# Kernel optimization log

Hardware: AMD Instinct MI355X
Metric: run time of the kernel (lower is better)

Reference implementation:

```python
import jax, jax.numpy as jnp
import numpy as np

ETA = 1.0
C_STAB = 0.1
SIGMA2 = 512.0  # RBF bandwidth, kernel_args['sigma2']
N_SAMPLE, S, D = 8192, 64, 512


def rbf_kernel(x, sigma2):
    # K[i,j] = exp(-||x_i - x_j||^2 / (2*sigma2)); x: [n, d] -> K: [n, n]
    sq = jnp.sum(x * x, axis=1)
    d2 = sq[:, None] + sq[None, :] - 2.0 * (x @ x.T)
    return jnp.exp(-d2 / (2.0 * sigma2))


def setup_inputs() -> dict:
    key = jax.random.key(0)
    k1, k2, k3 = jax.random.split(key, 3)
    return {
        "input_data": jax.random.normal(k1, (N_SAMPLE, D), dtype=jnp.float32),
        "weight": jax.random.normal(k2, (N_SAMPLE, S), dtype=jnp.float32),
        "inv_lambda_diag": jax.random.normal(k3, (S,), dtype=jnp.float32),
    }


def reference(input_data, weight, inv_lambda_diag):
    K = rbf_kernel(input_data, SIGMA2)          # [n, n]
    E = weight.T @ K                             # [s, n] : e_j for all samples at once
    # loss1 = sum_i e_i^T diag(inv_lambda) e_i, scaled
    loss1 = -jnp.sum(inv_lambda_diag[:, None] * E * E) / (2.0 * ETA ** 2)
    # loss2 = trace(W^T K W) = sum_{s,n} E[s,n] * W[n,s]
    loss2 = jnp.einsum("sn,ns->", E, weight) / (2.0 * ETA)
    L = loss1 + loss2
    return L + (C_STAB / 2.0) * jnp.square(L)
```

## Files before the change

### kernel.cpp

```cpp
#include <hip/hip_runtime.h>
#include <hip/hip_bf16.h>

typedef __bf16 bf16x8 __attribute__((ext_vector_type(8)));
typedef float f32x4 __attribute__((ext_vector_type(4)));
typedef long longx2 __attribute__((ext_vector_type(2)));

#define N 8192
#define D 512
#define NS 64

#define XS_OFF 0
#define WT_OFF (4 * 1024 * 1024)
#define SQ_OFF (WT_OFF + 1024 * 1024)
#define EP_OFF (SQ_OFF + 32 * 1024)
#define SC_OFF (EP_OFF + 8 * 64 * 8192 * 4)

__global__ __launch_bounds__(256) void prep(const float* __restrict__ X,
                                            const float* __restrict__ W,
                                            unsigned char* __restrict__ Xs,
                                            float* __restrict__ sq,
                                            __bf16* __restrict__ WTs,
                                            float* __restrict__ Sacc) {
    __shared__ float T[64][65];
    int t = threadIdx.x;
    if (blockIdx.x == 0 && t == 0) {
        Sacc[0] = 0.f; Sacc[1] = 0.f; ((int*)Sacc)[2] = 0;
    }
    if (blockIdx.x < 2048) {
        int row = blockIdx.x * 4 + (t >> 6);
        int l = t & 63;
        const float* src = X + (size_t)row * D + l * 8;
        float4 v0 = *(const float4*)src;
        float4 v1 = *(const float4*)(src + 4);
        int w0 = __builtin_amdgcn_cvt_pk_fp8_f32(v0.x, v0.y, 0, false);
        w0     = __builtin_amdgcn_cvt_pk_fp8_f32(v0.z, v0.w, w0, true);
        int w1 = __builtin_amdgcn_cvt_pk_fp8_f32(v1.x, v1.y, 0, false);
        w1     = __builtin_amdgcn_cvt_pk_fp8_f32(v1.z, v1.w, w1, true);
        int g = l >> 3, kh = (l >> 2) & 1, q = l & 3;
        int pos = g * 64 + q * 16 + kh * 8;
        uint2 pk = make_uint2((unsigned)w0, (unsigned)w1);
        *(uint2*)(Xs + (size_t)row * 512 + pos) = pk;
        float acc = v0.x*v0.x + v0.y*v0.y + v0.z*v0.z + v0.w*v0.w
                  + v1.x*v1.x + v1.y*v1.y + v1.z*v1.z + v1.w*v1.w;
        for (int off = 32; off > 0; off >>= 1) acc += __shfl_down(acc, off);
        if (l == 0) sq[row] = acc;
    } else {
        int i0 = (blockIdx.x - 2048) * 64;
        for (int j = 0; j < 16; ++j) {
            int idx = t + 256 * j;
            T[idx & 63][idx >> 6] = W[(size_t)(i0 + (idx >> 6)) * NS + (idx & 63)];
        }
        __syncthreads();
        for (int h = 0; h < 2; ++h)
            for (int j = 0; j < 8; ++j) {
                int idx = t + 256 * j;
                int s = idx >> 5, il = idx & 31;
                WTs[(size_t)((i0 >> 5) + h) * 2048 + idx] = (__bf16)T[s][h * 32 + il];
            }
    }
}

__global__ __launch_bounds__(256, 2) void kpca_main(
        const unsigned char* __restrict__ Xs, const __bf16* __restrict__ WTs,
        const float* __restrict__ sq, float* __restrict__ Ep) {
    __shared__ __align__(16) unsigned char Xi[2][8192];
    __shared__ __align__(16) unsigned char XnHi[128 * 272];
    __shared__ __align__(16) __bf16 KT[128 * 72];

    const int t = threadIdx.x;
    const int w = t >> 6, l = t & 63;
    const int quad = l >> 4, l15 = l & 15;
    const int wm = w >> 1, wn = w & 1;
    const int n0 = blockIdx.x * 128;
    const int ic0 = blockIdx.y * 1024;

    longx2 bc[4][4];
    {
        const unsigned char* Bb = Xs + (size_t)(n0 + wn * 64 + l15) * 512 + quad * 16;
        #pragma unroll
        for (int k8 = 0; k8 < 4; ++k8)
            #pragma unroll
            for (int nt = 0; nt < 4; ++nt)
                bc[k8][nt] = *(const longx2*)(Bb + nt * (16 * 512) + k8 * 64);
    }
    {
        int r = t >> 1, h = t & 1;
        const unsigned char* g = Xs + (size_t)(n0 + r) * 512 + 256 + h * 128;
        unsigned char* d = XnHi + r * 272 + h * 128;
        #pragma unroll
        for (int j = 0; j < 8; ++j)
            *(uint4*)(d + j * 16) = *(const uint4*)(g + j * 16);
    }
    float sqn_v[4];
    for (int nt = 0; nt < 4; ++nt)
        sqn_v[nt] = sq[n0 + wn * 64 + nt * 16 + l15];

    f32x4 accE[4][2];
    for (int st = 0; st < 4; ++st)
        for (int n2 = 0; n2 < 2; ++n2)
            accE[st][n2] = (f32x4){0.f, 0.f, 0.f, 0.f};

    const int ra = t >> 2, blk = (t & 3) * 16;

    {
        const unsigned char* g = Xs + (size_t)(ic0 + ra) * 512 + blk;
        *(uint4*)(Xi[0] + t * 16)        = *(const uint4*)g;
        *(uint4*)(Xi[0] + t * 16 + 4096) = *(const uint4*)(g + 64 * 512);
    }

    for (int it = 0; it < 8; ++it) {
        const int i0 = ic0 + it * 128;
        f32x4 accG[4][4];
        for (int mt = 0; mt < 4; ++mt)
            for (int nt = 0; nt < 4; ++nt)
                accG[mt][nt] = (f32x4){0.f, 0.f, 0.f, 0.f};

        #pragma unroll
        for (int kc8 = 0; kc8 < 8; ++kc8) {
            uint4 qA, qB;
            const bool stage = (kc8 < 7) || (it < 7);
            if (stage) {
                const int kn = (kc8 + 1) & 7;
                const int i0n = i0 + ((kc8 == 7) ? 128 : 0);
                const unsigned char* g = Xs + (size_t)(i0n + ra) * 512 + kn * 64 + blk;
                qA = *(const uint4*)g;
                qB = *(const uint4*)(g + 64 * 512);
            }
            __syncthreads();
            const unsigned char* xb = Xi[kc8 & 1];
            longx2 a[4], b[4];
            #pragma unroll
            for (int mt = 0; mt < 4; ++mt)
                a[mt] = *(const longx2*)(xb + (wm * 64 + mt * 16 + l15) * 64 + quad * 16);
            if (kc8 < 4) {
                #pragma unroll
                for (int nt = 0; nt < 4; ++nt) b[nt] = bc[kc8][nt];
            } else {
                #pragma unroll
                for (int nt = 0; nt < 4; ++nt)
                    b[nt] = *(const longx2*)(XnHi + (wn * 64 + nt * 16 + l15) * 272 +
                                             (kc8 - 4) * 64 + quad * 16);
            }
            #pragma unroll
            for (int mt = 0; mt < 4; ++mt)
                #pragma unroll
                for (int nt = 0; nt < 4; ++nt)
                    accG[mt][nt] = __builtin_amdgcn_mfma_f32_16x16x32_fp8_fp8(
                        a[mt][0], b[nt][0], accG[mt][nt], 0, 0, 0);
            #pragma unroll
            for (int mt = 0; mt < 4; ++mt)
                #pragma unroll
                for (int nt = 0; nt < 4; ++nt)
                    accG[mt][nt] = __builtin_amdgcn_mfma_f32_16x16x32_fp8_fp8(
                        a[mt][1], b[nt][1], accG[mt][nt], 0, 0, 0);
            if (stage) {
                unsigned char* xd = Xi[(kc8 + 1) & 1];
                *(uint4*)(xd + t * 16)        = qA;
                *(uint4*)(xd + t * 16 + 4096) = qB;
            }
        }

        uint2 pk[4][4];
        #pragma unroll
        for (int mt = 0; mt < 4; ++mt) {
            f32x4 si = *(const f32x4*)(sq + i0 + wm * 64 + mt * 16 + quad * 4);
            #pragma unroll
            for (int nt = 0; nt < 4; ++nt) {
                float sn = sqn_v[nt];
                union { __bf16 h[4]; uint2 u; } u;
                #pragma unroll
                for (int r = 0; r < 4; ++r) {
                    float d2 = si[r] + sn - 2.0f * accG[mt][nt][r];
                    u.h[r] = (__bf16)__expf(d2 * -9.765625e-4f);
                }
                pk[mt][nt] = u.u;
            }
        }

        const __bf16* wslab = WTs + (size_t)(i0 >> 5) * 2048;
        bf16x8 aw[2][4];
        #pragma unroll
        for (int kc2 = 0; kc2 < 2; ++kc2)
            for (int st = 0; st < 4; ++st)
                aw[kc2][st] = *(const bf16x8*)(wslab + kc2 * 2048 +
                                               (st * 16 + l15) * 32 + quad * 8);

        __syncthreads();
        if (wm == 0) {
            #pragma unroll
            for (int mt = 0; mt < 4; ++mt)
                for (int nt = 0; nt < 4; ++nt)
                    *(uint2*)(KT + (wn * 64 + nt * 16 + l15) * 72 + mt * 16 + quad * 4)
                        = pk[mt][nt];
        }
        __syncthreads();
        #pragma unroll
        for (int kc2 = 0; kc2 < 2; ++kc2) {
            bf16x8 bk[2];
            for (int n2 = 0; n2 < 2; ++n2)
                bk[n2] = *(const bf16x8*)(KT + (w * 32 + n2 * 16 + l15) * 72 +
                                          kc2 * 32 + quad * 8);
            #pragma unroll
            for (int st = 0; st < 4; ++st)
                for (int n2 = 0; n2 < 2; ++n2)
                    accE[st][n2] = __builtin_amdgcn_mfma_f32_16x16x32_bf16(
                        aw[kc2][st], bk[n2], accE[st][n2], 0, 0, 0);
        }
        #pragma unroll
        for (int kc2 = 0; kc2 < 2; ++kc2)
            for (int st = 0; st < 4; ++st)
                aw[kc2][st] = *(const bf16x8*)(wslab + (kc2 + 2) * 2048 +
                                               (st * 16 + l15) * 32 + quad * 8);
        __syncthreads();
        if (wm == 1) {
            #pragma unroll
            for (int mt = 0; mt < 4; ++mt)
                for (int nt = 0; nt < 4; ++nt)
                    *(uint2*)(KT + (wn * 64 + nt * 16 + l15) * 72 + mt * 16 + quad * 4)
                        = pk[mt][nt];
        }
        __syncthreads();
        #pragma unroll
        for (int kc2 = 0; kc2 < 2; ++kc2) {
            bf16x8 bk[2];
            for (int n2 = 0; n2 < 2; ++n2)
                bk[n2] = *(const bf16x8*)(KT + (w * 32 + n2 * 16 + l15) * 72 +
                                          kc2 * 32 + quad * 8);
            #pragma unroll
            for (int st = 0; st < 4; ++st)
                for (int n2 = 0; n2 < 2; ++n2)
                    accE[st][n2] = __builtin_amdgcn_mfma_f32_16x16x32_bf16(
                        aw[kc2][st], bk[n2], accE[st][n2], 0, 0, 0);
        }
    }

    float* ep = Ep + (size_t)blockIdx.y * (NS * N);
    #pragma unroll
    for (int st = 0; st < 4; ++st)
        for (int n2 = 0; n2 < 2; ++n2)
            for (int r = 0; r < 4; ++r) {
                int s = st * 16 + quad * 4 + r;
                int n = n0 + w * 32 + n2 * 16 + l15;
                ep[(size_t)s * N + n] = accE[st][n2][r];
            }
}

__global__ __launch_bounds__(256) void loss_kernel(const float* __restrict__ Ep,
                                                   const __bf16* __restrict__ WTs,
                                                   const float* __restrict__ lam,
                                                   float* __restrict__ Sacc,
                                                   float* __restrict__ out) {
    int s = blockIdx.x >> 2;
    int nb = (blockIdx.x & 3) * 2048;
    int t = threadIdx.x;
    float a1 = 0.f, a2 = 0.f;
    for (int j = 0; j < 8; ++j) {
        int n = nb + t + j * 256;
        float e = 0.f;
        #pragma unroll
        for (int c = 0; c < 8; ++c)
            e += Ep[(size_t)c * (NS * N) + (size_t)s * N + n];
        a1 += e * e;
        a2 += e * (float)WTs[(size_t)(n >> 5) * 2048 + s * 32 + (n & 31)];
    }
    for (int off = 32; off > 0; off >>= 1) {
        a1 += __shfl_down(a1, off);
        a2 += __shfl_down(a2, off);
    }
    __shared__ float r1[4], r2[4];
    int wv = t >> 6, ln = t & 63;
    if (ln == 0) { r1[wv] = a1; r2[wv] = a2; }
    __syncthreads();
    if (t == 0) {
        atomicAdd(Sacc + 0, lam[s] * (r1[0] + r1[1] + r1[2] + r1[3]));
        atomicAdd(Sacc + 1, r2[0] + r2[1] + r2[2] + r2[3]);
        __threadfence();
        int prev = atomicAdd((int*)Sacc + 2, 1);
        if (prev == 255) {
            __threadfence();
            volatile float* vs = (volatile float*)Sacc;
            float L = 0.5f * (vs[1] - vs[0]);
            out[0] = L + 0.05f * L * L;
        }
    }
}

extern "C" void kernel_launch(void* const* d_in, const int* in_sizes, int n_in,
                              void* d_out, int out_size, void* d_ws, size_t ws_size,
                              hipStream_t stream) {
    const float* X   = (const float*)d_in[0];
    const float* W   = (const float*)d_in[1];
    const float* lam = (const float*)d_in[2];
    float* out = (float*)d_out;
    char* ws = (char*)d_ws;
    unsigned char* Xs = (unsigned char*)(ws + XS_OFF);
    __bf16* WTs = (__bf16*)(ws + WT_OFF);
    float* sq   = (float*)(ws + SQ_OFF);
    float* Ep   = (float*)(ws + EP_OFF);
    float* Sacc = (float*)(ws + SC_OFF);

    prep<<<2048 + 128, 256, 0, stream>>>(X, W, Xs, sq, WTs, Sacc);
    kpca_main<<<dim3(64, 8), 256, 0, stream>>>(Xs, WTs, sq, Ep);
    loss_kernel<<<256, 256, 0, stream>>>(Ep, WTs, lam, Sacc, out);
}
```

Measured before the change: 146.5 us.

## Alias XnHi and KT in LDS, widen KT and halve per-tile barriers

XnHi (the upper half of the column operand) and the K-tile transpose buffer now share one LDS region. KT is widened to hold all 128 i-rows at once, so both warp rows write their exp tile together. This drops the two-phase write/consume sequence and two of the four barriers per outer iteration. Because KT overwrites XnHi, the upper X half is reloaded from global memory during the first four k-steps of every outer iteration. That adds repeated global/L2 traffic and extra registers in exchange for fewer syncs and a smaller LDS footprint.

```diff
diff --git a/kernel.cpp b/kernel.cpp
--- a/kernel.cpp
+++ b/kernel.cpp
@@ -64,8 +64,10 @@
         const unsigned char* __restrict__ Xs, const __bf16* __restrict__ WTs,
         const float* __restrict__ sq, float* __restrict__ Ep) {
     __shared__ __align__(16) unsigned char Xi[2][8192];
-    __shared__ __align__(16) unsigned char XnHi[128 * 272];
-    __shared__ __align__(16) __bf16 KT[128 * 72];
+    __shared__ __align__(16) unsigned char UN[128 * 272];
+
+    unsigned char* XnHi = UN;
+    __bf16* KT = (__bf16*)UN;
 
     const int t = threadIdx.x;
     const int w = t >> 6, l = t & 63;
@@ -83,14 +85,6 @@
             for (int nt = 0; nt < 4; ++nt)
                 bc[k8][nt] = *(const longx2*)(Bb + nt * (16 * 512) + k8 * 64);
     }
-    {
-        int r = t >> 1, h = t & 1;
-        const unsigned char* g = Xs + (size_t)(n0 + r) * 512 + 256 + h * 128;
-        unsigned char* d = XnHi + r * 272 + h * 128;
-        #pragma unroll
-        for (int j = 0; j < 8; ++j)
-            *(uint4*)(d + j * 16) = *(const uint4*)(g + j * 16);
-    }
     float sqn_v[4];
     for (int nt = 0; nt < 4; ++nt)
         sqn_v[nt] = sq[n0 + wn * 64 + nt * 16 + l15];
@@ -101,6 +95,9 @@
             accE[st][n2] = (f32x4){0.f, 0.f, 0.f, 0.f};
 
     const int ra = t >> 2, blk = (t & 3) * 16;
+    const int rr = t >> 1, hh = t & 1;
+    const unsigned char* rg = Xs + (size_t)(n0 + rr) * 512 + 256 + hh * 128;
+    unsigned char* rd = XnHi + rr * 272 + hh * 128;
 
     {
         const unsigned char* g = Xs + (size_t)(ic0 + ra) * 512 + blk;
@@ -126,6 +123,11 @@
                 qA = *(const uint4*)g;
                 qB = *(const uint4*)(g + 64 * 512);
             }
+            uint4 rv0, rv1;
+            if (kc8 < 4) {
+                rv0 = *(const uint4*)(rg + kc8 * 32);
+                rv1 = *(const uint4*)(rg + kc8 * 32 + 16);
+            }
             __syncthreads();
             const unsigned char* xb = Xi[kc8 & 1];
             longx2 a[4], b[4];
@@ -158,6 +160,10 @@
                 *(uint4*)(xd + t * 16)        = qA;
                 *(uint4*)(xd + t * 16 + 4096) = qB;
             }
+            if (kc8 < 4) {
+                *(uint4*)(rd + kc8 * 32)      = rv0;
+                *(uint4*)(rd + kc8 * 32 + 16) = rv1;
+            }
         }
 
         uint2 pk[4][4];
@@ -186,19 +192,20 @@
                                                (st * 16 + l15) * 32 + quad * 8);
 
         __syncthreads();
-        if (wm == 0) {
-            #pragma unroll
-            for (int mt = 0; mt < 4; ++mt)
-                for (int nt = 0; nt < 4; ++nt)
-                    *(uint2*)(KT + (wn * 64 + nt * 16 + l15) * 72 + mt * 16 + quad * 4)
-                        = pk[mt][nt];
+        #pragma unroll
+        for (int mt = 0; mt < 4; ++mt) {
+            const int ibase = wm * 64 + mt * 16 + quad * 4;
+            #pragma unroll
+            for (int nt = 0; nt < 4; ++nt)
+                *(uint2*)(KT + (wn * 64 + nt * 16 + l15) * 136 + ibase) = pk[mt][nt];
         }
         __syncthreads();
+
         #pragma unroll
         for (int kc2 = 0; kc2 < 2; ++kc2) {
             bf16x8 bk[2];
             for (int n2 = 0; n2 < 2; ++n2)
-                bk[n2] = *(const bf16x8*)(KT + (w * 32 + n2 * 16 + l15) * 72 +
+                bk[n2] = *(const bf16x8*)(KT + (w * 32 + n2 * 16 + l15) * 136 +
                                           kc2 * 32 + quad * 8);
             #pragma unroll
             for (int st = 0; st < 4; ++st)
@@ -211,21 +218,12 @@
             for (int st = 0; st < 4; ++st)
                 aw[kc2][st] = *(const bf16x8*)(wslab + (kc2 + 2) * 2048 +
                                                (st * 16 + l15) * 32 + quad * 8);
-        __syncthreads();
-        if (wm == 1) {
-            #pragma unroll
-            for (int mt = 0; mt < 4; ++mt)
-                for (int nt = 0; nt < 4; ++nt)
-                    *(uint2*)(KT + (wn * 64 + nt * 16 + l15) * 72 + mt * 16 + quad * 4)
-                        = pk[mt][nt];
-        }
-        __syncthreads();
         #pragma unroll
         for (int kc2 = 0; kc2 < 2; ++kc2) {
             bf16x8 bk[2];
             for (int n2 = 0; n2 < 2; ++n2)
-                bk[n2] = *(const bf16x8*)(KT + (w * 32 + n2 * 16 + l15) * 72 +
-                                          kc2 * 32 + quad * 8);
+                bk[n2] = *(const bf16x8*)(KT + (w * 32 + n2 * 16 + l15) * 136 +
+                                          (kc2 + 2) * 32 + quad * 8);
             #pragma unroll
             for (int st = 0; st < 4; ++st)
                 for (int n2 = 0; n2 < 2; ++n2)
```

After: 173.3 us. +18.3%, slower.
